# Optimization experiments

Hardware: AMD Instinct MI355X
Metric: run time of the kernel (lower is better)

## Reference

```python
import jax, jax.numpy as jnp
import numpy as np

IN_FEATURES = 8192
OUT_FEATURES = 14336
M_TOKENS = 64


def _dequant_rowwise_int4(w_packed, w_scales):
    # w_packed: [out, in//2], each byte holds two signed int4 values
    # (low nibble = even k index, high nibble = odd k index, two's complement)
    low = w_packed & 0xF
    high = (w_packed >> 4) & 0xF
    q = jnp.stack([low, high], axis=-1).reshape(w_packed.shape[0], -1)  # [out, in]
    q = jnp.where(q >= 8, q - 16, q).astype(jnp.float32)
    return q * w_scales[:, None]  # [out, in]


def setup_inputs() -> dict:
    key = jax.random.key(0)
    k1, k2, k3, k4 = jax.random.split(key, 4)
    x = jax.random.normal(k1, (M_TOKENS, IN_FEATURES), dtype=jnp.float32)
    w_packed = jax.random.randint(k2, (OUT_FEATURES, IN_FEATURES // 2), 0, 256, dtype=jnp.int32)
    # per-row scales, small positive values as produced by max-abs/7 quantization
    w_scales = jax.random.uniform(k3, (OUT_FEATURES,), dtype=jnp.float32) * 0.02 + 1e-4
    bias = jax.random.normal(k4, (OUT_FEATURES,), dtype=jnp.float32)
    return {"x": x, "w_packed": w_packed, "w_scales": w_scales, "bias": bias}


def reference(x, w_packed, w_scales, bias):
    original_shape = x.shape[:-1]
    x_2d = x.reshape(-1, IN_FEATURES)
    w = _dequant_rowwise_int4(w_packed, w_scales)  # [out, in]
    y = x_2d @ w.T + bias[None, :]  # [M, out]
    return y.reshape(*original_shape, OUT_FEATURES)
```

## Files before the change

kernel.cpp:

```cpp
#include <hip/hip_runtime.h>

#define IN_F   8192
#define OUT_F  14336
#define M_TOK  64
#define KPI    4096
#define BN     128
#define NBLK   (OUT_F / BN)
#define KSPLIT 8
#define KCHUNK (IN_F / KSPLIT)
#define BK     128
#define NSTEP  (KCHUNK / BK)

typedef __attribute__((ext_vector_type(8)))  short bf16x8;
typedef __attribute__((ext_vector_type(16))) float f32x16;

__device__ __forceinline__ unsigned short f2bf_rne(float f) {
    unsigned u = __builtin_bit_cast(unsigned, f);
    u += 0x7FFFu + ((u >> 16) & 1u);
    return (unsigned short)(u >> 16);
}

__global__ __launch_bounds__(256) void qlin_prep(const float* __restrict__ x,
                                                 const float* __restrict__ bias,
                                                 unsigned short* __restrict__ xb,
                                                 float* __restrict__ out) {
    const int XV = (M_TOK * IN_F) / 4;
    const int OV = (M_TOK * OUT_F) / 4;
    int gid = blockIdx.x * 256 + threadIdx.x;
    if (gid < XV) {
        float4 v = reinterpret_cast<const float4*>(x)[gid];
        ushort4 o;
        o.x = f2bf_rne(v.x);
        o.y = f2bf_rne(v.y);
        o.z = f2bf_rne(v.z);
        o.w = f2bf_rne(v.w);
        reinterpret_cast<ushort4*>(xb)[gid] = o;
    } else {
        int og = gid - XV;
        if (og < OV) {
            float4 b = reinterpret_cast<const float4*>(bias)[og % (OUT_F / 4)];
            reinterpret_cast<float4*>(out)[og] = b;
        }
    }
}

__device__ __forceinline__ int unpack2_bf16(int v) {
    int q0 = ((int)((unsigned)v << 28)) >> 28;
    int q1 = ((int)((unsigned)v << 24)) >> 28;
    unsigned u0 = __builtin_bit_cast(unsigned, (float)q0);
    unsigned u1 = __builtin_bit_cast(unsigned, (float)q1);
    return (int)((u0 >> 16) | (u1 & 0xFFFF0000u));
}

__device__ __forceinline__ bf16x8 unpack_b(int4 wv) {
    int4 pk;
    pk.x = unpack2_bf16(wv.x);
    pk.y = unpack2_bf16(wv.y);
    pk.z = unpack2_bf16(wv.z);
    pk.w = unpack2_bf16(wv.w);
    return __builtin_bit_cast(bf16x8, pk);
}

__device__ __forceinline__ void gload_lds16(const void* g, void* l) {
    __builtin_amdgcn_global_load_lds(
        (const __attribute__((address_space(1))) unsigned int*)g,
        (__attribute__((address_space(3))) unsigned int*)l,
        16, 0, 0);
}

__global__ __launch_bounds__(256) void qlin_gemm(const unsigned short* __restrict__ xb,
                                                 const int* __restrict__ wp,
                                                 const float* __restrict__ scales,
                                                 float* __restrict__ out) {
    __shared__ int            wlds[BN * (BK / 2)];
    __shared__ unsigned short xlds[M_TOK * BK];

    const int tid  = threadIdx.x;
    const int wave = tid >> 6;
    const int lane = tid & 63;
    const int tp   = lane & 31;
    const int qp   = lane >> 5;

    const int nblk = blockIdx.x % NBLK;
    const int kblk = blockIdx.x / NBLK;
    const int n0   = nblk * BN;
    const int kb   = kblk * KCHUNK;

    f32x16 acc0 = {0.f,0.f,0.f,0.f,0.f,0.f,0.f,0.f,0.f,0.f,0.f,0.f,0.f,0.f,0.f,0.f};
    f32x16 acc1 = acc0;

    for (int step = 0; step < NSTEP; ++step) {
#pragma unroll
        for (int j = 0; j < 8; ++j) {
            int li = (wave * 8 + j) * 64 + lane;
            int r  = li >> 4;
            int c  = li & 15;
            const int* gp = wp + (size_t)(n0 + r) * KPI + (kb >> 1) + step * (BK / 2) + c * 4;
            gload_lds16(gp, (char*)wlds + (size_t)li * 16);
        }
#pragma unroll
        for (int j = 0; j < 4; ++j) {
            int li = (wave * 4 + j) * 64 + lane;
            int r  = li >> 4;
            int c  = li & 15;
            const unsigned short* gp = xb + (size_t)r * IN_F + kb + step * BK + c * 8;
            gload_lds16(gp, (char*)xlds + (size_t)li * 16);
        }
        __syncthreads();

#pragma unroll
        for (int kf = 0; kf < 8; ++kf) {
            int4 wv = *reinterpret_cast<const int4*>(
                (const char*)wlds + ((wave * 32 + tp) * (BK / 2) + kf * 8 + qp * 4) * 4);
            bf16x8 b  = unpack_b(wv);
            bf16x8 a0 = *reinterpret_cast<const bf16x8*>(
                (const char*)xlds + ((tp)      * BK + kf * 16 + qp * 8) * 2);
            bf16x8 a1 = *reinterpret_cast<const bf16x8*>(
                (const char*)xlds + ((32 + tp) * BK + kf * 16 + qp * 8) * 2);
            acc0 = __builtin_amdgcn_mfma_f32_32x32x16_bf16(a0, b, acc0, 0, 0, 0);
            acc1 = __builtin_amdgcn_mfma_f32_32x32x16_bf16(a1, b, acc1, 0, 0, 0);
        }
        __syncthreads();
    }

    const int   n  = n0 + wave * 32 + tp;
    const float sc = scales[n];
#pragma unroll
    for (int reg = 0; reg < 16; ++reg) {
        int m = (reg & 3) + 8 * (reg >> 2) + 4 * qp;
        atomicAdd(&out[(size_t)m        * OUT_F + n], acc0[reg] * sc);
        atomicAdd(&out[(size_t)(32 + m) * OUT_F + n], acc1[reg] * sc);
    }
}

extern "C" void kernel_launch(void* const* d_in, const int* in_sizes, int n_in,
                              void* d_out, int out_size, void* d_ws, size_t ws_size,
                              hipStream_t stream) {
    const float* x    = (const float*)d_in[0];
    const int*   wp   = (const int*)d_in[1];
    const float* sc   = (const float*)d_in[2];
    const float* bias = (const float*)d_in[3];
    float* out = (float*)d_out;
    unsigned short* xb = (unsigned short*)d_ws;

    const int prep_items = (M_TOK * IN_F) / 4 + (M_TOK * OUT_F) / 4;
    qlin_prep<<<(prep_items + 255) / 256, 256, 0, stream>>>(x, bias, xb, out);
    qlin_gemm<<<NBLK * KSPLIT, 256, 0, stream>>>(xb, wp, sc, out);
}
```

Measured before the change: 358.2 us.

## Replace atomic split-K with partial buffers, XOR-swizzled LDS, smaller BK and more splits

Each K-split block now writes its scaled partial tile to its own workspace slice, and a separate reduce kernel sums the slices and adds bias. This replaces the global float atomics. The split factor doubles, BK halves and launch bounds request more resident blocks, giving more parallelism and smaller LDS tiles. LDS tiles also get an XOR swizzle to cut bank conflicts. The cost is extra global traffic: 16 partial output slices written and read back, about 59 MB, plus a third kernel launch.

After: 355.9 us. About the same (-0.6%).

```diff
diff --git a/kernel.cpp b/kernel.cpp
--- a/kernel.cpp
+++ b/kernel.cpp
@@ -6,10 +6,11 @@
 #define KPI    4096
 #define BN     128
 #define NBLK   (OUT_F / BN)
-#define KSPLIT 8
+#define KSPLIT 16
 #define KCHUNK (IN_F / KSPLIT)
-#define BK     128
+#define BK     64
 #define NSTEP  (KCHUNK / BK)
+#define PSTRIDE (M_TOK * OUT_F)
 
 typedef __attribute__((ext_vector_type(8)))  short bf16x8;
 typedef __attribute__((ext_vector_type(16))) float f32x16;
@@ -21,27 +22,15 @@
 }
 
 __global__ __launch_bounds__(256) void qlin_prep(const float* __restrict__ x,
-                                                 const float* __restrict__ bias,
-                                                 unsigned short* __restrict__ xb,
-                                                 float* __restrict__ out) {
-    const int XV = (M_TOK * IN_F) / 4;
-    const int OV = (M_TOK * OUT_F) / 4;
+                                                 unsigned short* __restrict__ xb) {
     int gid = blockIdx.x * 256 + threadIdx.x;
-    if (gid < XV) {
-        float4 v = reinterpret_cast<const float4*>(x)[gid];
-        ushort4 o;
-        o.x = f2bf_rne(v.x);
-        o.y = f2bf_rne(v.y);
-        o.z = f2bf_rne(v.z);
-        o.w = f2bf_rne(v.w);
-        reinterpret_cast<ushort4*>(xb)[gid] = o;
-    } else {
-        int og = gid - XV;
-        if (og < OV) {
-            float4 b = reinterpret_cast<const float4*>(bias)[og % (OUT_F / 4)];
-            reinterpret_cast<float4*>(out)[og] = b;
-        }
-    }
+    float4 v = reinterpret_cast<const float4*>(x)[gid];
+    ushort4 o;
+    o.x = f2bf_rne(v.x);
+    o.y = f2bf_rne(v.y);
+    o.z = f2bf_rne(v.z);
+    o.w = f2bf_rne(v.w);
+    reinterpret_cast<ushort4*>(xb)[gid] = o;
 }
 
 __device__ __forceinline__ int unpack2_bf16(int v) {
@@ -68,10 +57,10 @@
         16, 0, 0);
 }
 
-__global__ __launch_bounds__(256) void qlin_gemm(const unsigned short* __restrict__ xb,
-                                                 const int* __restrict__ wp,
-                                                 const float* __restrict__ scales,
-                                                 float* __restrict__ out) {
+__global__ __launch_bounds__(256, 6) void qlin_gemm(const unsigned short* __restrict__ xb,
+                                                    const int* __restrict__ wp,
+                                                    const float* __restrict__ scales,
+                                                    float* __restrict__ part) {
     __shared__ int            wlds[BN * (BK / 2)];
     __shared__ unsigned short xlds[M_TOK * BK];
 
@@ -91,32 +80,34 @@
 
     for (int step = 0; step < NSTEP; ++step) {
 #pragma unroll
-        for (int j = 0; j < 8; ++j) {
-            int li = (wave * 8 + j) * 64 + lane;
-            int r  = li >> 4;
-            int c  = li & 15;
-            const int* gp = wp + (size_t)(n0 + r) * KPI + (kb >> 1) + step * (BK / 2) + c * 4;
+        for (int j = 0; j < 4; ++j) {
+            int li = (wave * 4 + j) * 64 + lane;
+            int r  = li >> 3;
+            int cg = (li & 7) ^ (r & 7);
+            const int* gp = wp + (size_t)(n0 + r) * KPI + (kb >> 1) + step * (BK / 2) + cg * 4;
             gload_lds16(gp, (char*)wlds + (size_t)li * 16);
         }
 #pragma unroll
-        for (int j = 0; j < 4; ++j) {
-            int li = (wave * 4 + j) * 64 + lane;
-            int r  = li >> 4;
-            int c  = li & 15;
-            const unsigned short* gp = xb + (size_t)r * IN_F + kb + step * BK + c * 8;
+        for (int j = 0; j < 2; ++j) {
+            int li = (wave * 2 + j) * 64 + lane;
+            int r  = li >> 3;
+            int cg = (li & 7) ^ (r & 7);
+            const unsigned short* gp = xb + (size_t)r * IN_F + kb + step * BK + cg * 8;
             gload_lds16(gp, (char*)xlds + (size_t)li * 16);
         }
         __syncthreads();
 
 #pragma unroll
-        for (int kf = 0; kf < 8; ++kf) {
+        for (int kf = 0; kf < 4; ++kf) {
+            const int c = kf * 2 + qp;
+            const int R = wave * 32 + tp;
             int4 wv = *reinterpret_cast<const int4*>(
-                (const char*)wlds + ((wave * 32 + tp) * (BK / 2) + kf * 8 + qp * 4) * 4);
+                (const char*)wlds + (size_t)(R * 8 + (c ^ (R & 7))) * 16);
             bf16x8 b  = unpack_b(wv);
             bf16x8 a0 = *reinterpret_cast<const bf16x8*>(
-                (const char*)xlds + ((tp)      * BK + kf * 16 + qp * 8) * 2);
+                (const char*)xlds + (size_t)(tp * 8 + (c ^ (tp & 7))) * 16);
             bf16x8 a1 = *reinterpret_cast<const bf16x8*>(
-                (const char*)xlds + ((32 + tp) * BK + kf * 16 + qp * 8) * 2);
+                (const char*)xlds + (size_t)((32 + tp) * 8 + (c ^ (tp & 7))) * 16);
             acc0 = __builtin_amdgcn_mfma_f32_32x32x16_bf16(a0, b, acc0, 0, 0, 0);
             acc1 = __builtin_amdgcn_mfma_f32_32x32x16_bf16(a1, b, acc1, 0, 0, 0);
         }
@@ -125,12 +116,26 @@
 
     const int   n  = n0 + wave * 32 + tp;
     const float sc = scales[n];
+    float* p = part + (size_t)kblk * PSTRIDE;
 #pragma unroll
     for (int reg = 0; reg < 16; ++reg) {
         int m = (reg & 3) + 8 * (reg >> 2) + 4 * qp;
-        atomicAdd(&out[(size_t)m        * OUT_F + n], acc0[reg] * sc);
-        atomicAdd(&out[(size_t)(32 + m) * OUT_F + n], acc1[reg] * sc);
+        p[(size_t)m        * OUT_F + n] = acc0[reg] * sc;
+        p[(size_t)(32 + m) * OUT_F + n] = acc1[reg] * sc;
     }
+}
+
+__global__ __launch_bounds__(256) void qlin_reduce(const float* __restrict__ part,
+                                                   const float* __restrict__ bias,
+                                                   float* __restrict__ out) {
+    int g = blockIdx.x * 256 + threadIdx.x;
+    float4 acc = reinterpret_cast<const float4*>(bias)[g % (OUT_F / 4)];
+#pragma unroll
+    for (int s = 0; s < KSPLIT; ++s) {
+        float4 v = reinterpret_cast<const float4*>(part + (size_t)s * PSTRIDE)[g];
+        acc.x += v.x; acc.y += v.y; acc.z += v.z; acc.w += v.w;
+    }
+    reinterpret_cast<float4*>(out)[g] = acc;
 }
 
 extern "C" void kernel_launch(void* const* d_in, const int* in_sizes, int n_in,
@@ -141,9 +146,11 @@
     const float* sc   = (const float*)d_in[2];
     const float* bias = (const float*)d_in[3];
     float* out = (float*)d_out;
-    unsigned short* xb = (unsigned short*)d_ws;
 
-    const int prep_items = (M_TOK * IN_F) / 4 + (M_TOK * OUT_F) / 4;
-    qlin_prep<<<(prep_items + 255) / 256, 256, 0, stream>>>(x, bias, xb, out);
-    qlin_gemm<<<NBLK * KSPLIT, 256, 0, stream>>>(xb, wp, sc, out);
+    unsigned short* xb   = (unsigned short*)d_ws;
+    float*          part = (float*)((char*)d_ws + (1 << 20));
+
+    qlin_prep<<<(M_TOK * IN_F) / 4 / 256, 256, 0, stream>>>(x, xb);
+    qlin_gemm<<<NBLK * KSPLIT, 256, 0, stream>>>(xb, wp, sc, part);
+    qlin_reduce<<<(M_TOK * OUT_F) / 4 / 256, 256, 0, stream>>>(part, bias, out);
 }
```

## Replace split-K atomic GEMM with full-K row blocks and in-block wave reduction

Applied to the files above, without the earlier changes.

Each block now owns 64 output columns across the full K range, so split-K and the float atomics into the output go away. Weight slabs are double-buffered through registers into LDS, while activations are pre-swizzled by the prep kernel into MFMA fragment order and read straight from global memory. The four waves split K within each slab and are reduced through LDS, and scale and bias are applied in the epilogue. The grid drops to 224 blocks, which risks low occupancy and poor latency hiding on a large-CU GPU, and every block rereads all of x from global or L2.

After: 427.2 us. 1.19x slower.

```diff
diff --git a/kernel.cpp b/kernel.cpp
--- a/kernel.cpp
+++ b/kernel.cpp
@@ -3,16 +3,15 @@
 #define IN_F   8192
 #define OUT_F  14336
 #define M_TOK  64
-#define KPI    4096
-#define BN     128
-#define NBLK   (OUT_F / BN)
-#define KSPLIT 8
-#define KCHUNK (IN_F / KSPLIT)
-#define BK     128
-#define NSTEP  (KCHUNK / BK)
+#define ROWB   64
+#define NBLK   (OUT_F / ROWB)
+#define SLABK  256
+#define NSLAB  (IN_F / SLABK)
+#define WROWB  512
 
-typedef __attribute__((ext_vector_type(8)))  short bf16x8;
-typedef __attribute__((ext_vector_type(16))) float f32x16;
+typedef __attribute__((ext_vector_type(8))) short          bf16x8;
+typedef __attribute__((ext_vector_type(8))) unsigned short u16x8;
+typedef __attribute__((ext_vector_type(4))) float          f32x4;
 
 __device__ __forceinline__ unsigned short f2bf_rne(float f) {
     unsigned u = __builtin_bit_cast(unsigned, f);
@@ -21,27 +20,17 @@
 }
 
 __global__ __launch_bounds__(256) void qlin_prep(const float* __restrict__ x,
-                                                 const float* __restrict__ bias,
-                                                 unsigned short* __restrict__ xb,
-                                                 float* __restrict__ out) {
-    const int XV = (M_TOK * IN_F) / 4;
-    const int OV = (M_TOK * OUT_F) / 4;
-    int gid = blockIdx.x * 256 + threadIdx.x;
-    if (gid < XV) {
-        float4 v = reinterpret_cast<const float4*>(x)[gid];
-        ushort4 o;
-        o.x = f2bf_rne(v.x);
-        o.y = f2bf_rne(v.y);
-        o.z = f2bf_rne(v.z);
-        o.w = f2bf_rne(v.w);
-        reinterpret_cast<ushort4*>(xb)[gid] = o;
-    } else {
-        int og = gid - XV;
-        if (og < OV) {
-            float4 b = reinterpret_cast<const float4*>(bias)[og % (OUT_F / 4)];
-            reinterpret_cast<float4*>(out)[og] = b;
-        }
-    }
+                                                 unsigned short* __restrict__ xs) {
+    int tid  = blockIdx.x * 256 + threadIdx.x;
+    int lane = tid & 63;
+    int mt   = (tid >> 6) & 3;
+    int fg   = tid >> 8;
+    int q = lane >> 4, t = lane & 15;
+    const float* src = x + (size_t)(mt * 16 + t) * IN_F + fg * 32 + q * 8;
+    u16x8 o;
+#pragma unroll
+    for (int j = 0; j < 8; ++j) o[j] = f2bf_rne(src[j]);
+    *reinterpret_cast<u16x8*>(xs + (size_t)tid * 8) = o;
 }
 
 __device__ __forceinline__ int unpack2_bf16(int v) {
@@ -61,75 +50,96 @@
     return __builtin_bit_cast(bf16x8, pk);
 }
 
-__device__ __forceinline__ void gload_lds16(const void* g, void* l) {
-    __builtin_amdgcn_global_load_lds(
-        (const __attribute__((address_space(1))) unsigned int*)g,
-        (__attribute__((address_space(3))) unsigned int*)l,
-        16, 0, 0);
-}
-
-__global__ __launch_bounds__(256) void qlin_gemm(const unsigned short* __restrict__ xb,
+__global__ __launch_bounds__(256) void qlin_gemm(const unsigned short* __restrict__ xs,
                                                  const int* __restrict__ wp,
                                                  const float* __restrict__ scales,
+                                                 const float* __restrict__ bias,
                                                  float* __restrict__ out) {
-    __shared__ int            wlds[BN * (BK / 2)];
-    __shared__ unsigned short xlds[M_TOK * BK];
+    __shared__ int wl[2][ROWB * WROWB / 4];
 
     const int tid  = threadIdx.x;
     const int wave = tid >> 6;
     const int lane = tid & 63;
-    const int tp   = lane & 31;
-    const int qp   = lane >> 5;
+    const int t = lane & 15;
+    const int q = lane >> 4;
+    const int n0 = blockIdx.x * ROWB;
 
-    const int nblk = blockIdx.x % NBLK;
-    const int kblk = blockIdx.x / NBLK;
-    const int n0   = nblk * BN;
-    const int kb   = kblk * KCHUNK;
+    const char* wpb = (const char*)wp;
+    const int srow = 2 * wave * 8 + (lane >> 5);
+    const int scol = (lane & 31) * 16;
 
-    f32x16 acc0 = {0.f,0.f,0.f,0.f,0.f,0.f,0.f,0.f,0.f,0.f,0.f,0.f,0.f,0.f,0.f,0.f};
-    f32x16 acc1 = acc0;
+    f32x4 acc[4][4] = {};
 
-    for (int step = 0; step < NSTEP; ++step) {
+    int4 g[8];
 #pragma unroll
-        for (int j = 0; j < 8; ++j) {
-            int li = (wave * 8 + j) * 64 + lane;
-            int r  = li >> 4;
-            int c  = li & 15;
-            const int* gp = wp + (size_t)(n0 + r) * KPI + (kb >> 1) + step * (BK / 2) + c * 4;
-            gload_lds16(gp, (char*)wlds + (size_t)li * 16);
+    for (int j = 0; j < 8; ++j)
+        g[j] = *reinterpret_cast<const int4*>(
+            wpb + (size_t)(n0 + srow + 2 * j) * 16384 + scol);
+#pragma unroll
+    for (int j = 0; j < 8; ++j)
+        *reinterpret_cast<int4*>((char*)wl[0] + (srow + 2 * j) * WROWB + scol) = g[j];
+    __syncthreads();
+
+    for (int s = 0; s < NSLAB; ++s) {
+        const int buf = s & 1;
+        if (s + 1 < NSLAB) {
+#pragma unroll
+            for (int j = 0; j < 8; ++j)
+                g[j] = *reinterpret_cast<const int4*>(
+                    wpb + (size_t)(n0 + srow + 2 * j) * 16384 + (size_t)(s + 1) * WROWB + scol);
         }
 #pragma unroll
-        for (int j = 0; j < 4; ++j) {
-            int li = (wave * 4 + j) * 64 + lane;
-            int r  = li >> 4;
-            int c  = li & 15;
-            const unsigned short* gp = xb + (size_t)r * IN_F + kb + step * BK + c * 8;
-            gload_lds16(gp, (char*)xlds + (size_t)li * 16);
+        for (int f = 0; f < 2; ++f) {
+            bf16x8 a[4];
+            const int fg = s * 8 + wave * 2 + f;
+#pragma unroll
+            for (int mt = 0; mt < 4; ++mt)
+                a[mt] = *reinterpret_cast<const bf16x8*>(
+                    xs + ((size_t)(fg * 4 + mt) * 64 + lane) * 8);
+#pragma unroll
+            for (int nt = 0; nt < 4; ++nt) {
+                int4 wv = *reinterpret_cast<const int4*>(
+                    (const char*)wl[buf] + (nt * 16 + t) * WROWB + wave * 128 + f * 64 + q * 16);
+                bf16x8 b = unpack_b(wv);
+#pragma unroll
+                for (int mt = 0; mt < 4; ++mt)
+                    acc[nt][mt] = __builtin_amdgcn_mfma_f32_16x16x32_bf16(
+                        a[mt], b, acc[nt][mt], 0, 0, 0);
+            }
         }
-        __syncthreads();
-
+        if (s + 1 < NSLAB) {
 #pragma unroll
-        for (int kf = 0; kf < 8; ++kf) {
-            int4 wv = *reinterpret_cast<const int4*>(
-                (const char*)wlds + ((wave * 32 + tp) * (BK / 2) + kf * 8 + qp * 4) * 4);
-            bf16x8 b  = unpack_b(wv);
-            bf16x8 a0 = *reinterpret_cast<const bf16x8*>(
-                (const char*)xlds + ((tp)      * BK + kf * 16 + qp * 8) * 2);
-            bf16x8 a1 = *reinterpret_cast<const bf16x8*>(
-                (const char*)xlds + ((32 + tp) * BK + kf * 16 + qp * 8) * 2);
-            acc0 = __builtin_amdgcn_mfma_f32_32x32x16_bf16(a0, b, acc0, 0, 0, 0);
-            acc1 = __builtin_amdgcn_mfma_f32_32x32x16_bf16(a1, b, acc1, 0, 0, 0);
+            for (int j = 0; j < 8; ++j)
+                *reinterpret_cast<int4*>(
+                    (char*)wl[buf ^ 1] + (srow + 2 * j) * WROWB + scol) = g[j];
         }
         __syncthreads();
     }
 
-    const int   n  = n0 + wave * 32 + tp;
-    const float sc = scales[n];
+    float* red = (float*)wl;
 #pragma unroll
-    for (int reg = 0; reg < 16; ++reg) {
-        int m = (reg & 3) + 8 * (reg >> 2) + 4 * qp;
-        atomicAdd(&out[(size_t)m        * OUT_F + n], acc0[reg] * sc);
-        atomicAdd(&out[(size_t)(32 + m) * OUT_F + n], acc1[reg] * sc);
+    for (int nt = 0; nt < 4; ++nt)
+#pragma unroll
+        for (int mt = 0; mt < 4; ++mt)
+#pragma unroll
+            for (int r = 0; r < 4; ++r)
+                red[wave * 4096 + (nt * 16 + t) * 64 + mt * 16 + q * 4 + r] =
+                    acc[nt][mt][r];
+    __syncthreads();
+
+    const int m  = tid >> 2;
+    const int ng = (tid & 3) * 16;
+#pragma unroll
+    for (int i = 0; i < 16; i += 4) {
+        float4 v;
+#pragma unroll
+        for (int c = 0; c < 4; ++c) {
+            const int nl = ng + i + c;
+            float sum = red[0 * 4096 + nl * 64 + m] + red[1 * 4096 + nl * 64 + m]
+                      + red[2 * 4096 + nl * 64 + m] + red[3 * 4096 + nl * 64 + m];
+            v[c] = sum * scales[n0 + nl] + bias[n0 + nl];
+        }
+        *reinterpret_cast<float4*>(out + (size_t)m * OUT_F + n0 + ng + i) = v;
     }
 }
 
@@ -141,9 +151,8 @@
     const float* sc   = (const float*)d_in[2];
     const float* bias = (const float*)d_in[3];
     float* out = (float*)d_out;
-    unsigned short* xb = (unsigned short*)d_ws;
+    unsigned short* xs = (unsigned short*)d_ws;
 
-    const int prep_items = (M_TOK * IN_F) / 4 + (M_TOK * OUT_F) / 4;
-    qlin_prep<<<(prep_items + 255) / 256, 256, 0, stream>>>(x, bias, xb, out);
-    qlin_gemm<<<NBLK * KSPLIT, 256, 0, stream>>>(xb, wp, sc, out);
+    qlin_prep<<<256, 256, 0, stream>>>(x, xs);
+    qlin_gemm<<<NBLK, 256, 0, stream>>>(xs, wp, sc, bias, out);
 }
```
